# Performance work log

Hardware: AMD Instinct MI355X
Metric: run time of the kernel (lower is better)

The kernel has to match this reference:

```python
import jax, jax.numpy as jnp
import numpy as np

N = 50000      # nodes (full graph: num_dst == num_src == N)
E = 800000     # edges, avg degree 16
D = 128        # in_feats == n_hidden == out_feats
L = 3          # n_layers
EPS = 1e-5     # BatchNorm1d eps


def setup_inputs() -> dict:
    key = jax.random.key(0)
    ks = jax.random.split(key, 6)
    feat = jax.random.normal(ks[0], (N, D), dtype=jnp.float32)
    src = jax.random.randint(ks[1], (E,), 0, N)
    dst = jax.random.randint(ks[2], (E,), 0, N)
    scale = 1.0 / np.sqrt(D)
    W_self = jax.random.normal(ks[3], (L, D, D), dtype=jnp.float32) * scale
    W_neigh = jax.random.normal(ks[4], (L, D, D), dtype=jnp.float32) * scale
    b = jax.random.normal(ks[5], (L, D), dtype=jnp.float32) * 0.01
    gamma = jnp.ones((L - 1, D), dtype=jnp.float32)
    beta = jnp.zeros((L - 1, D), dtype=jnp.float32)
    return {"feat": feat, "src": src, "dst": dst, "W_self": W_self,
            "W_neigh": W_neigh, "b": b, "gamma": gamma, "beta": beta}


def reference(feat, src, dst, W_self, W_neigh, b, gamma, beta):
    n = feat.shape[0]
    n_layers = W_self.shape[0]
    # in-degree of each dst node, clamped to 1 (zero-degree nodes aggregate 0)
    deg = jax.ops.segment_sum(jnp.ones_like(dst, dtype=feat.dtype), dst,
                              num_segments=n)
    deg = jnp.maximum(deg, 1.0)[:, None]                      # [N,1]
    h = feat
    for i in range(n_layers):
        # mean aggregation over incoming neighbors: gather + segment-sum
        agg = jax.ops.segment_sum(h[src], dst, num_segments=n) / deg  # [N,D]
        # SAGEConv('mean'): fc_self(h_dst) + fc_neigh(agg) + bias
        hn = h @ W_self[i] + agg @ W_neigh[i] + b[i]
        hn = hn + h                                           # residual (dims match)
        if i < n_layers - 1:
            mu = jnp.mean(hn, axis=0)
            var = jnp.var(hn, axis=0)                         # biased, as BN training
            hn = (hn - mu) * jax.lax.rsqrt(var + EPS) * gamma[i] + beta[i]
            hn = jax.nn.relu(hn)
        h = hn
    return h
```

## Files before the change

### kernel.cpp

```cpp
#include <hip/hip_runtime.h>

#define DIM 128
#define EPSF 1e-5f
#define BK_SHIFT 10
#define BK_NODES 1024
#define BK_CAP 20480

typedef __attribute__((ext_vector_type(8))) short short8;
typedef __attribute__((ext_vector_type(4))) float float4v;

__device__ inline unsigned short f2bf(float x) {
    union { float f; unsigned u; } z; z.f = x;
    unsigned u = z.u;
    unsigned r = u + 0x7FFF + ((u >> 16) & 1);
    return (unsigned short)(r >> 16);
}
__device__ inline float bf2f(unsigned short u) {
    union { unsigned u; float f; } z; z.u = ((unsigned)u) << 16;
    return z.f;
}

__global__ void binA_kernel(const int* __restrict__ src, const int* __restrict__ dst,
                            unsigned* __restrict__ barr, int* __restrict__ bcnt,
                            int E, int NB) {
    __shared__ int cnt[64];
    __shared__ int gcur[64];
    int tid = threadIdx.x;
    int tile0 = blockIdx.x * 4096;
    if (tid < 64) cnt[tid] = 0;
    __syncthreads();
    unsigned pk[16]; int bk[16];
#pragma unroll
    for (int i = 0; i < 16; ++i) {
        int e = tile0 + i * 256 + tid;
        if (e < E) {
            int d = dst[e];
            int s = src[e];
            bk[i] = d >> BK_SHIFT;
            pk[i] = ((unsigned)(d & (BK_NODES - 1)) << 16) | (unsigned)s;
            atomicAdd(&cnt[bk[i]], 1);
        } else bk[i] = -1;
    }
    __syncthreads();
    if (tid < 64) {
        int c = (tid < NB) ? cnt[tid] : 0;
        gcur[tid] = (c > 0) ? atomicAdd(&bcnt[tid], c) : 0;
    }
    __syncthreads();
#pragma unroll
    for (int i = 0; i < 16; ++i) {
        if (bk[i] >= 0) {
            int pos = atomicAdd(&gcur[bk[i]], 1);
            if (pos < BK_CAP)
                barr[(size_t)bk[i] * BK_CAP + pos] = pk[i];
        }
    }
}

__global__ void bucketscan_kernel(const int* __restrict__ bcnt, int* __restrict__ bbase,
                                  int NB, int* __restrict__ rowptr, int N, int E) {
    if (threadIdx.x == 0) {
        int run = 0;
        for (int b = 0; b < NB; ++b) { bbase[b] = run; run += bcnt[b]; }
        rowptr[N] = E;
    }
}

__global__ void binB_kernel(const unsigned* __restrict__ barr, const int* __restrict__ bcnt,
                            const int* __restrict__ bbase, int* __restrict__ rowptr,
                            int* __restrict__ colidx, int N) {
    __shared__ int hist[BK_NODES];
    __shared__ int sm[256];
    int b = blockIdx.x;
    int tid = threadIdx.x;
    int cnt = bcnt[b];
    if (cnt > BK_CAP) cnt = BK_CAP;
    const unsigned* arr = barr + (size_t)b * BK_CAP;
    int gb = bbase[b];
#pragma unroll
    for (int j = 0; j < 4; ++j) hist[tid * 4 + j] = 0;
    __syncthreads();
    for (int i = tid; i < cnt; i += 256)
        atomicAdd(&hist[arr[i] >> 16], 1);
    __syncthreads();
    int h[4], s = 0;
#pragma unroll
    for (int j = 0; j < 4; ++j) { h[j] = hist[tid * 4 + j]; s += h[j]; }
    sm[tid] = s;
    __syncthreads();
    int tot = s;
    for (int off = 1; off < 256; off <<= 1) {
        int x = (tid >= off) ? sm[tid - off] : 0;
        __syncthreads();
        sm[tid] += x;
        __syncthreads();
    }
    int run = sm[tid] - tot;
#pragma unroll
    for (int j = 0; j < 4; ++j) { hist[tid * 4 + j] = run; run += h[j]; }
    __syncthreads();
    int nbase = b << BK_SHIFT;
    int nn = N - nbase; if (nn > BK_NODES) nn = BK_NODES;
    for (int j = tid; j < nn; j += 256)
        rowptr[nbase + j] = gb + hist[j];
    __syncthreads();
    for (int i = tid; i < cnt; i += 256) {
        unsigned u = arr[i];
        int pos = atomicAdd(&hist[u >> 16], 1);
        colidx[gb + pos] = (int)(u & 0xFFFFu);
    }
}

__global__ void packw_kernel(const float* __restrict__ Ws, const float* __restrict__ Wn,
                             unsigned short* __restrict__ wpack) {
    int l = blockIdx.x >> 3;
    int s = blockIdx.x & 7;
    int tid = threadIdx.x;
#pragma unroll
    for (int pi = 0; pi < 2; ++pi) {
        int p = tid * 2 + pi;
        int nt = p >> 6;
        int lane = p & 63;
        int kb = s * 32 + (lane >> 4) * 8;
        int col = nt * 16 + (lane & 15);
        unsigned short* dstp = wpack + (size_t)l * 32768 + ((size_t)(s * 8 + nt) * 64 + lane) * 8;
#pragma unroll
        for (int j = 0; j < 8; ++j) {
            int k = kb + j;
            float v = (k < 128) ? Ws[(size_t)l * 16384 + k * 128 + col]
                                : Wn[(size_t)l * 16384 + (k - 128) * 128 + col];
            dstp[j] = f2bf(v);
        }
    }
}

__global__ void convert_kernel(const float* __restrict__ feat, unsigned short* __restrict__ Acat,
                               int N) {
    int idx = blockIdx.x * blockDim.x + threadIdx.x;
    if (idx >= N * 32) return;
    float4 v = ((const float4*)feat)[idx];
    int r = idx >> 5, c4 = idx & 31;
    ushort4 o;
    o.x = f2bf(v.x); o.y = f2bf(v.y); o.z = f2bf(v.z); o.w = f2bf(v.w);
    ((ushort4*)Acat)[(size_t)r * 64 + c4] = o;
}

__global__ void aggregate_kernel(unsigned short* Acat, const int* __restrict__ rowptr,
                                 const int* __restrict__ colidx, int N) {
    int wid = (blockIdx.x * blockDim.x + threadIdx.x) >> 6;
    if (wid >= N) return;
    int lane = threadIdx.x & 63;
    int half = lane >> 5, sl = lane & 31;
    int beg = rowptr[wid], end = rowptr[wid + 1];
    float4 acc = make_float4(0.f, 0.f, 0.f, 0.f);
    int e = beg + half;
    for (; e + 2 < end; e += 4) {
        int s0 = colidx[e];
        int s1 = colidx[e + 2];
        ushort4 u0 = *(const ushort4*)(Acat + (size_t)s0 * 256 + sl * 4);
        ushort4 u1 = *(const ushort4*)(Acat + (size_t)s1 * 256 + sl * 4);
        acc.x += bf2f(u0.x) + bf2f(u1.x);
        acc.y += bf2f(u0.y) + bf2f(u1.y);
        acc.z += bf2f(u0.z) + bf2f(u1.z);
        acc.w += bf2f(u0.w) + bf2f(u1.w);
    }
    if (e < end) {
        int s0 = colidx[e];
        ushort4 u0 = *(const ushort4*)(Acat + (size_t)s0 * 256 + sl * 4);
        acc.x += bf2f(u0.x);
        acc.y += bf2f(u0.y);
        acc.z += bf2f(u0.z);
        acc.w += bf2f(u0.w);
    }
    acc.x += __shfl_xor(acc.x, 32);
    acc.y += __shfl_xor(acc.y, 32);
    acc.z += __shfl_xor(acc.z, 32);
    acc.w += __shfl_xor(acc.w, 32);
    if (half == 0) {
        int deg = end - beg;
        float inv = 1.0f / (float)(deg > 0 ? deg : 1);
        ushort4 o;
        o.x = f2bf(acc.x * inv); o.y = f2bf(acc.y * inv);
        o.z = f2bf(acc.z * inv); o.w = f2bf(acc.w * inv);
        *(ushort4*)(Acat + (size_t)wid * 256 + 128 + sl * 4) = o;
    }
}

__launch_bounds__(256)
__global__ void gemm_kernel(const unsigned short* __restrict__ Acat,
                            const unsigned short* __restrict__ wpack,
                            const float* __restrict__ hres, const float* __restrict__ bias,
                            float* __restrict__ out, float* __restrict__ stats,
                            int withStats, int N) {
    __shared__ unsigned short Bs[32768];
    int tid = threadIdx.x;
    {
        const float4* wsrc = (const float4*)wpack;
        float4* bdst = (float4*)Bs;
#pragma unroll
        for (int i = 0; i < 16; ++i) bdst[i * 256 + tid] = wsrc[i * 256 + tid];
    }
    __syncthreads();

    int wave = tid >> 6, lane = tid & 63;
    int row0 = blockIdx.x * 128 + wave * 32;
    int mrow = lane & 15, kq = lane >> 4;
    const unsigned short* Abase = Acat + (size_t)(row0 + mrow) * 256 + kq * 8;

    float4v acc[2][8];
#pragma unroll
    for (int i = 0; i < 2; ++i)
#pragma unroll
        for (int j = 0; j < 8; ++j) acc[i][j] = (float4v){0.f, 0.f, 0.f, 0.f};

#pragma unroll
    for (int s = 0; s < 8; ++s) {
        short8 a0 = *(const short8*)(Abase + s * 32);
        short8 a1 = *(const short8*)(Abase + 16 * 256 + s * 32);
#pragma unroll
        for (int nt = 0; nt < 8; ++nt) {
            short8 b = *(const short8*)(Bs + ((size_t)(s * 8 + nt) * 64 + lane) * 8);
            acc[0][nt] = __builtin_amdgcn_mfma_f32_16x16x32_bf16(a0, b, acc[0][nt], 0, 0, 0);
            acc[1][nt] = __builtin_amdgcn_mfma_f32_16x16x32_bf16(a1, b, acc[1][nt], 0, 0, 0);
        }
    }

    float* sm = (float*)Bs;
    if (withStats) {
        __syncthreads();
        sm[tid] = 0.f;
        __syncthreads();
    }

    int colb = lane & 15;
    int rq = (lane >> 4) * 4;
#pragma unroll
    for (int mt = 0; mt < 2; ++mt) {
        int rowt = row0 + mt * 16 + rq;
#pragma unroll
        for (int nt = 0; nt < 8; ++nt) {
            int col = nt * 16 + colb;
            float bv = bias[col];
            float slo = 0.f, qlo = 0.f;
#pragma unroll
            for (int r = 0; r < 4; ++r) {
                int row = rowt + r;
                if (row < N) {
                    float v = acc[mt][nt][r] + bv + hres[(size_t)row * 128 + col];
                    out[(size_t)row * 128 + col] = v;
                    slo += v; qlo += v * v;
                }
            }
            if (withStats) {
                atomicAdd(&sm[col], slo);
                atomicAdd(&sm[128 + col], qlo);
            }
        }
    }
    if (withStats) {
        __syncthreads();
        if (tid < 128) {
            atomicAdd(&stats[tid], sm[tid]);
            atomicAdd(&stats[128 + tid], sm[128 + tid]);
        }
    }
}

__global__ void bnprep_kernel(const float* __restrict__ stats, const float* __restrict__ gamma,
                              const float* __restrict__ beta, float* __restrict__ scsh, int N) {
    int t = threadIdx.x;
    if (t >= 128) return;
    float invN = 1.0f / (float)N;
    float mean = stats[t] * invN;
    float var = stats[128 + t] * invN - mean * mean;
    float sc = gamma[t] * rsqrtf(var + EPSF);
    scsh[t] = sc;
    scsh[128 + t] = beta[t] - mean * sc;
}

__global__ void bnapply_kernel(float* __restrict__ io, unsigned short* __restrict__ Acat,
                               const float* __restrict__ scsh, int N) {
    int idx = blockIdx.x * blockDim.x + threadIdx.x;
    if (idx >= N * 32) return;
    float4 v = ((float4*)io)[idx];
    int c4 = idx & 31;
    float4 sc = ((const float4*)scsh)[c4];
    float4 sh = ((const float4*)(scsh + 128))[c4];
    v.x = fmaxf(fmaf(v.x, sc.x, sh.x), 0.f);
    v.y = fmaxf(fmaf(v.y, sc.y, sh.y), 0.f);
    v.z = fmaxf(fmaf(v.z, sc.z, sh.z), 0.f);
    v.w = fmaxf(fmaf(v.w, sc.w, sh.w), 0.f);
    ((float4*)io)[idx] = v;
    ushort4 o;
    o.x = f2bf(v.x); o.y = f2bf(v.y); o.z = f2bf(v.z); o.w = f2bf(v.w);
    ((ushort4*)Acat)[(size_t)(idx >> 5) * 64 + c4] = o;
}

extern "C" void kernel_launch(void* const* d_in, const int* in_sizes, int n_in,
                              void* d_out, int out_size, void* d_ws, size_t ws_size,
                              hipStream_t stream) {
    const float* feat  = (const float*)d_in[0];
    const int*   src   = (const int*)d_in[1];
    const int*   dst   = (const int*)d_in[2];
    const float* Wself = (const float*)d_in[3];
    const float* Wneig = (const float*)d_in[4];
    const float* bias  = (const float*)d_in[5];
    const float* gamma = (const float*)d_in[6];
    const float* beta  = (const float*)d_in[7];

    int N = in_sizes[0] / DIM;
    int E = in_sizes[1];
    int Npad = (N + 127) & ~127;
    int NB = (N + BK_NODES - 1) >> BK_SHIFT;

    char* ws = (char*)d_ws;
    size_t off = 0;
    auto alloc = [&](size_t bytes) -> void* {
        void* p = ws + off;
        off = (off + bytes + 255) & ~(size_t)255;
        return p;
    };
    float*          hF     = (float*)alloc((size_t)Npad * DIM * 4);
    unsigned short* Acat   = (unsigned short*)alloc((size_t)Npad * 256 * 2);
    unsigned short* wpack  = (unsigned short*)alloc((size_t)3 * 32768 * 2);
    int*   colidx = (int*)alloc((size_t)E * 4);
    int*   rowptr = (int*)alloc((size_t)(N + 1) * 4);
    int*   bcnt   = (int*)alloc(64 * 4);
    int*   bbase  = (int*)alloc(64 * 4);
    float* stats  = (float*)alloc(256 * 4);
    float* scsh   = (float*)alloc(256 * 4);

    unsigned* barr = (unsigned*)Acat;

    hipMemsetAsync(bcnt, 0, 64 * 4, stream);
    binA_kernel<<<(E + 4095) / 4096, 256, 0, stream>>>(src, dst, barr, bcnt, E, NB);
    bucketscan_kernel<<<1, 64, 0, stream>>>(bcnt, bbase, NB, rowptr, N, E);
    binB_kernel<<<NB, 256, 0, stream>>>(barr, bcnt, bbase, rowptr, colidx, N);

    packw_kernel<<<24, 256, 0, stream>>>(Wself, Wneig, wpack);
    convert_kernel<<<(N * 32 + 255) / 256, 256, 0, stream>>>(feat, Acat, N);
    if (Npad > N)
        hipMemsetAsync(Acat + (size_t)N * 256, 0, (size_t)(Npad - N) * 512, stream);

    const float* hres[3] = { feat, hF, hF };
    float* houts[3] = { hF, hF, (float*)d_out };

    for (int l = 0; l < 3; ++l) {
        aggregate_kernel<<<(N + 3) / 4, 256, 0, stream>>>(Acat, rowptr, colidx, N);
        int withStats = (l < 2) ? 1 : 0;
        if (withStats) hipMemsetAsync(stats, 0, 256 * 4, stream);
        gemm_kernel<<<Npad / 128, 256, 0, stream>>>(
            Acat, wpack + (size_t)l * 32768, hres[l], bias + (size_t)l * DIM,
            houts[l], stats, withStats, N);
        if (withStats) {
            bnprep_kernel<<<1, 128, 0, stream>>>(stats, gamma + (size_t)l * DIM,
                                                 beta + (size_t)l * DIM, scsh, N);
            bnapply_kernel<<<(N * 32 + 255) / 256, 256, 0, stream>>>(houts[l], Acat, scsh, N);
        }
    }
}
```

Before: 383.7 us.

## Store intermediate activations in bf16 and fuse BN prep into apply

```diff
diff --git a/kernel.cpp b/kernel.cpp
--- a/kernel.cpp
+++ b/kernel.cpp
@@ -7,6 +7,7 @@
 #define BK_CAP 20480
 
 typedef __attribute__((ext_vector_type(8))) short short8;
+typedef __attribute__((ext_vector_type(8))) unsigned short ushort8;
 typedef __attribute__((ext_vector_type(4))) float float4v;
 
 __device__ inline unsigned short f2bf(float x) {
@@ -189,9 +190,9 @@
 __launch_bounds__(256)
 __global__ void gemm_kernel(const unsigned short* __restrict__ Acat,
                             const unsigned short* __restrict__ wpack,
-                            const float* __restrict__ hres, const float* __restrict__ bias,
-                            float* __restrict__ out, float* __restrict__ stats,
-                            int withStats, int N) {
+                            const float* __restrict__ bias,
+                            unsigned short* __restrict__ outb, float* __restrict__ outf,
+                            float* __restrict__ stats, int withStats, int N) {
     __shared__ unsigned short Bs[32768];
     int tid = threadIdx.x;
     {
@@ -246,9 +247,14 @@
             for (int r = 0; r < 4; ++r) {
                 int row = rowt + r;
                 if (row < N) {
-                    float v = acc[mt][nt][r] + bv + hres[(size_t)row * 128 + col];
-                    out[(size_t)row * 128 + col] = v;
-                    slo += v; qlo += v * v;
+                    float res = bf2f(Acat[(size_t)row * 256 + col]);
+                    float v = acc[mt][nt][r] + bv + res;
+                    if (withStats) {
+                        outb[(size_t)row * 128 + col] = f2bf(v);
+                        slo += v; qlo += v * v;
+                    } else {
+                        outf[(size_t)row * 128 + col] = v;
+                    }
                 }
             }
             if (withStats) {
@@ -266,34 +272,37 @@
     }
 }
 
-__global__ void bnprep_kernel(const float* __restrict__ stats, const float* __restrict__ gamma,
-                              const float* __restrict__ beta, float* __restrict__ scsh, int N) {
-    int t = threadIdx.x;
-    if (t >= 128) return;
-    float invN = 1.0f / (float)N;
-    float mean = stats[t] * invN;
-    float var = stats[128 + t] * invN - mean * mean;
-    float sc = gamma[t] * rsqrtf(var + EPSF);
-    scsh[t] = sc;
-    scsh[128 + t] = beta[t] - mean * sc;
-}
-
-__global__ void bnapply_kernel(float* __restrict__ io, unsigned short* __restrict__ Acat,
-                               const float* __restrict__ scsh, int N) {
-    int idx = blockIdx.x * blockDim.x + threadIdx.x;
+__global__ void bnapply_kernel(const unsigned short* __restrict__ hn,
+                               unsigned short* __restrict__ Acat,
+                               const float* __restrict__ stats, const float* __restrict__ gamma,
+                               const float* __restrict__ beta, float invN, int N) {
+    __shared__ float sc_s[128], sh_s[128];
+    int tid = threadIdx.x;
+    if (tid < 128) {
+        float mean = stats[tid] * invN;
+        float var = stats[128 + tid] * invN - mean * mean;
+        float sc = gamma[tid] * rsqrtf(var + EPSF);
+        sc_s[tid] = sc;
+        sh_s[tid] = beta[tid] - mean * sc;
+    }
+    __syncthreads();
+    int idx = blockIdx.x * 256 + tid;
     if (idx >= N * 32) return;
-    float4 v = ((float4*)io)[idx];
-    int c4 = idx & 31;
-    float4 sc = ((const float4*)scsh)[c4];
-    float4 sh = ((const float4*)(scsh + 128))[c4];
-    v.x = fmaxf(fmaf(v.x, sc.x, sh.x), 0.f);
-    v.y = fmaxf(fmaf(v.y, sc.y, sh.y), 0.f);
-    v.z = fmaxf(fmaf(v.z, sc.z, sh.z), 0.f);
-    v.w = fmaxf(fmaf(v.w, sc.w, sh.w), 0.f);
-    ((float4*)io)[idx] = v;
+    int row = idx >> 5, c4 = idx & 31;
+    ushort4 u = *(const ushort4*)(hn + (size_t)idx * 4);
     ushort4 o;
-    o.x = f2bf(v.x); o.y = f2bf(v.y); o.z = f2bf(v.z); o.w = f2bf(v.w);
-    ((ushort4*)Acat)[(size_t)(idx >> 5) * 64 + c4] = o;
+    {
+        int col = c4 * 4;
+        float v0 = fmaf(bf2f(u.x), sc_s[col], sh_s[col]);
+        float v1 = fmaf(bf2f(u.y), sc_s[col + 1], sh_s[col + 1]);
+        float v2 = fmaf(bf2f(u.z), sc_s[col + 2], sh_s[col + 2]);
+        float v3 = fmaf(bf2f(u.w), sc_s[col + 3], sh_s[col + 3]);
+        o.x = f2bf(fmaxf(v0, 0.f));
+        o.y = f2bf(fmaxf(v1, 0.f));
+        o.z = f2bf(fmaxf(v2, 0.f));
+        o.w = f2bf(fmaxf(v3, 0.f));
+    }
+    *(ushort4*)(Acat + (size_t)row * 256 + c4 * 4) = o;
 }
 
 extern "C" void kernel_launch(void* const* d_in, const int* in_sizes, int n_in,
@@ -320,15 +329,14 @@
         off = (off + bytes + 255) & ~(size_t)255;
         return p;
     };
-    float*          hF     = (float*)alloc((size_t)Npad * DIM * 4);
     unsigned short* Acat   = (unsigned short*)alloc((size_t)Npad * 256 * 2);
+    unsigned short* hnS    = (unsigned short*)alloc((size_t)Npad * 128 * 2);
     unsigned short* wpack  = (unsigned short*)alloc((size_t)3 * 32768 * 2);
     int*   colidx = (int*)alloc((size_t)E * 4);
     int*   rowptr = (int*)alloc((size_t)(N + 1) * 4);
     int*   bcnt   = (int*)alloc(64 * 4);
     int*   bbase  = (int*)alloc(64 * 4);
     float* stats  = (float*)alloc(256 * 4);
-    float* scsh   = (float*)alloc(256 * 4);
 
     unsigned* barr = (unsigned*)Acat;
 
@@ -342,20 +350,17 @@
     if (Npad > N)
         hipMemsetAsync(Acat + (size_t)N * 256, 0, (size_t)(Npad - N) * 512, stream);
 
-    const float* hres[3] = { feat, hF, hF };
-    float* houts[3] = { hF, hF, (float*)d_out };
+    float invN = 1.0f / (float)N;
 
     for (int l = 0; l < 3; ++l) {
         aggregate_kernel<<<(N + 3) / 4, 256, 0, stream>>>(Acat, rowptr, colidx, N);
         int withStats = (l < 2) ? 1 : 0;
         if (withStats) hipMemsetAsync(stats, 0, 256 * 4, stream);
         gemm_kernel<<<Npad / 128, 256, 0, stream>>>(
-            Acat, wpack + (size_t)l * 32768, hres[l], bias + (size_t)l * DIM,
-            houts[l], stats, withStats, N);
-        if (withStats) {
-            bnprep_kernel<<<1, 128, 0, stream>>>(stats, gamma + (size_t)l * DIM,
-                                                 beta + (size_t)l * DIM, scsh, N);
-            bnapply_kernel<<<(N * 32 + 255) / 256, 256, 0, stream>>>(houts[l], Acat, scsh, N);
-        }
-    }
-}
+            Acat, wpack + (size_t)l * 32768, bias + (size_t)l * DIM,
+            hnS, (float*)d_out, stats, withStats, N);
+        if (withStats)
+            bnapply_kernel<<<(N * 32 + 255) / 256, 256, 0, stream>>>(
+                hnS, Acat, stats, gamma + (size_t)l * DIM, beta + (size_t)l * DIM, invN, N);
+    }
+}
```

Result: faster. 364.5 us (-5.0%).
